# Performance work log

Measured on AMD Instinct MI355X. Metric: run time of the kernel, lower is better.

The kernel has to match this reference:

```python
import jax, jax.numpy as jnp
import numpy as np

HEAD_NUM = 16
EMBED_DIM = 1024
HIDDEN_DIM = 1024
HEAD_DIM = HIDDEN_DIM // HEAD_NUM


def setup_inputs() -> dict:
    key = jax.random.key(0)
    ks = jax.random.split(key, 7)
    B, S = 2, 2048
    X = jax.random.normal(ks[0], (B, S, EMBED_DIM), dtype=jnp.float32)
    sc = 1.0 / np.sqrt(EMBED_DIM)
    Wq = jax.random.normal(ks[1], (EMBED_DIM, HIDDEN_DIM), dtype=jnp.float32) * sc
    Wk = jax.random.normal(ks[2], (EMBED_DIM, HIDDEN_DIM), dtype=jnp.float32) * sc
    Wv = jax.random.normal(ks[3], (EMBED_DIM, HIDDEN_DIM), dtype=jnp.float32) * sc
    bq = jax.random.normal(ks[4], (HIDDEN_DIM,), dtype=jnp.float32) * 0.01
    bk = jax.random.normal(ks[5], (HIDDEN_DIM,), dtype=jnp.float32) * 0.01
    bv = jax.random.normal(ks[6], (HIDDEN_DIM,), dtype=jnp.float32) * 0.01
    return {"X": X, "Wq": Wq, "bq": bq, "Wk": Wk, "bk": bk, "Wv": Wv, "bv": bv}


def reference(X, Wq, bq, Wk, bk, Wv, bv):
    B, S, _ = X.shape
    # projections -> [B, H, S, D]
    def split_heads(t):
        return t.reshape(B, S, HEAD_NUM, HEAD_DIM).transpose(0, 2, 1, 3)
    Q = split_heads(X @ Wq + bq)
    K = split_heads(X @ Wk + bk)  # computed but unused, faithful to source bug
    V = split_heads(X @ Wv + bv)
    # NOTE: source computes Q @ V^T (bug), reproduced faithfully
    scores = jnp.einsum('bhqd,bhkd->bhqk', Q, V) / np.sqrt(HEAD_DIM)
    attn = jax.nn.softmax(scores, axis=-1)  # dropout is identity in eval
    out = jnp.einsum('bhqk,bhkd->bhqd', attn, V)
    return out.transpose(0, 2, 1, 3).reshape(B, S, HIDDEN_DIM)
```

## Files before the change

kernel.cpp:

```cpp
#include <hip/hip_runtime.h>
#include <math.h>


constexpr int BATCH = 2;
constexpr int SEQ   = 2048;
constexpr int EMB   = 1024;
constexpr int NHEAD = 16;
constexpr int HDIM  = 64;
constexpr int HID   = 1024;

typedef __attribute__((ext_vector_type(8))) _Float16 half8;
typedef __attribute__((ext_vector_type(4))) float    f32x4;

#define MFMA16(a, b, c) __builtin_amdgcn_mfma_f32_16x16x32_f16((a), (b), (c), 0, 0, 0)

constexpr int LDT = 80;

__device__ __forceinline__ _Float16 f2h(float f) { return (_Float16)f; }

__global__ __launch_bounds__(256) void conv_x_kernel(
    const float* __restrict__ X, _Float16* __restrict__ Xb, int n4)
{
    union Pack { uint2 q; _Float16 e[4]; };
    int idx = blockIdx.x * 256 + threadIdx.x;
    int stride = gridDim.x * 256;
    for (int i = idx; i < n4; i += stride) {
        float4 v = ((const float4*)X)[i];
        Pack p;
        p.e[0] = f2h(v.x); p.e[1] = f2h(v.y);
        p.e[2] = f2h(v.z); p.e[3] = f2h(v.w);
        ((uint2*)Xb)[i] = p.q;
    }
}

__global__ __launch_bounds__(256) void conv_wt_kernel(
    const float* __restrict__ W, _Float16* __restrict__ WT)
{
    __shared__ _Float16 T[64 * 68];
    const int tid = threadIdx.x;
    const int n0 = blockIdx.x * 64;
    const int k0 = blockIdx.y * 64;

    #pragma unroll
    for (int i = 0; i < 4; ++i) {
        const int u = tid + i * 256;
        const int r = u >> 4;
        const int c4 = (u & 15) << 2;
        const float4 v = *(const float4*)&W[(size_t)(k0 + r) * HID + n0 + c4];
        T[r * 68 + c4 + 0] = f2h(v.x);
        T[r * 68 + c4 + 1] = f2h(v.y);
        T[r * 68 + c4 + 2] = f2h(v.z);
        T[r * 68 + c4 + 3] = f2h(v.w);
    }
    __syncthreads();

    union Pack { uint4 q; _Float16 e[8]; };
    #pragma unroll
    for (int i = 0; i < 2; ++i) {
        const int u = tid + i * 256;
        const int n = u >> 3;
        const int kc = (u & 7) << 3;
        Pack p;
        #pragma unroll
        for (int j = 0; j < 8; ++j) p.e[j] = T[(kc + j) * 68 + n];
        *(uint4*)&WT[(size_t)(n0 + n) * EMB + k0 + kc] = p.q;
    }
}

__global__ __launch_bounds__(256) void proj_kernel(
    const _Float16* __restrict__ Xb, const _Float16* __restrict__ WTq,
    const _Float16* __restrict__ WTv, const float* __restrict__ bq,
    const float* __restrict__ bv, _Float16* __restrict__ Qo,
    _Float16* __restrict__ Vo, _Float16* __restrict__ VTo)
{
    __shared__ __align__(16) _Float16 Xs[128 * LDT];
    __shared__ __align__(16) _Float16 Wqs[64 * LDT];
    __shared__ __align__(16) _Float16 Wvs[64 * LDT];

    const int tid  = threadIdx.x;
    const int lane = tid & 63;
    const int w    = tid >> 6;
    const int wg   = blockIdx.x;
    const int nid  = (wg & 7) * 64 + (wg >> 3);
    const int h    = nid >> 5;
    const int m0   = (nid & 31) * 128;
    const int n0   = h * HDIM;
    const int l15  = lane & 15;
    const int l4   = lane >> 4;

    f32x4 aq[2][4], av[2][4];
    #pragma unroll
    for (int mt = 0; mt < 2; ++mt)
        #pragma unroll
        for (int nt = 0; nt < 4; ++nt) {
            aq[mt][nt] = f32x4{0.f, 0.f, 0.f, 0.f};
            av[mt][nt] = f32x4{0.f, 0.f, 0.f, 0.f};
        }

    for (int k0 = 0; k0 < EMB; k0 += 64) {
        #pragma unroll
        for (int i = 0; i < 4; ++i) {
            const int u = tid + i * 256;
            const int r = u >> 3;
            const int c8 = (u & 7) << 3;
            *(uint4*)&Xs[r * LDT + c8] =
                *(const uint4*)&Xb[(size_t)(m0 + r) * EMB + k0 + c8];
        }
        #pragma unroll
        for (int i = 0; i < 2; ++i) {
            const int u = tid + i * 256;
            const int r = u >> 3;
            const int c8 = (u & 7) << 3;
            *(uint4*)&Wqs[r * LDT + c8] =
                *(const uint4*)&WTq[(size_t)(n0 + r) * EMB + k0 + c8];
            *(uint4*)&Wvs[r * LDT + c8] =
                *(const uint4*)&WTv[(size_t)(n0 + r) * EMB + k0 + c8];
        }
        __syncthreads();

        __builtin_amdgcn_s_setprio(1);
        #pragma unroll
        for (int kd = 0; kd < 2; ++kd) {
            const int ko = kd * 32 + l4 * 8;
            half8 xa0 = *(const half8*)&Xs[(w * 32 + l15) * LDT + ko];
            half8 xa1 = *(const half8*)&Xs[(w * 32 + 16 + l15) * LDT + ko];
            #pragma unroll
            for (int nt = 0; nt < 4; ++nt) {
                half8 wq = *(const half8*)&Wqs[(nt * 16 + l15) * LDT + ko];
                half8 wv = *(const half8*)&Wvs[(nt * 16 + l15) * LDT + ko];
                aq[0][nt] = MFMA16(xa0, wq, aq[0][nt]);
                aq[1][nt] = MFMA16(xa1, wq, aq[1][nt]);
                av[0][nt] = MFMA16(xa0, wv, av[0][nt]);
                av[1][nt] = MFMA16(xa1, wv, av[1][nt]);
            }
        }
        __builtin_amdgcn_s_setprio(0);
        __syncthreads();
    }

    #pragma unroll
    for (int nt = 0; nt < 4; ++nt) {
        const int d = nt * 16 + l15;
        const float bqv = bq[n0 + d];
        const float bvv = bv[n0 + d];
        #pragma unroll
        for (int mt = 0; mt < 2; ++mt)
            #pragma unroll
            for (int r = 0; r < 4; ++r) {
                const int m = m0 + w * 32 + mt * 16 + l4 * 4 + r;
                const int bb = m >> 11;
                const int s  = m & (SEQ - 1);
                const int bh = bb * NHEAD + h;
                const float vval = av[mt][nt][r] + bvv;
                Qo[((size_t)bh * SEQ + s) * HDIM + d] = f2h(aq[mt][nt][r] + bqv);
                Vo[((size_t)bh * SEQ + s) * HDIM + d] = f2h(vval);
                VTo[((size_t)bh * HDIM + d) * SEQ + s] = f2h(vval);
            }
    }
}

__global__ __launch_bounds__(256) void attn_kernel(
    const _Float16* __restrict__ Qw, const _Float16* __restrict__ Vw,
    const _Float16* __restrict__ VTw, float* __restrict__ out)
{
    __shared__ __align__(16) _Float16 PQs[64 * LDT];
    __shared__ __align__(16) _Float16 Vs[64 * LDT];
    __shared__ __align__(16) _Float16 VTs[64 * LDT];

    const int tid  = threadIdx.x;
    const int lane = tid & 63;
    const int w    = tid >> 6;
    const int l15  = lane & 15;
    const int l4   = lane >> 4;
    const int wg = blockIdx.x;
    const int nw = (wg & 7) * 128 + (wg >> 3);
    const int bh = nw >> 5;
    const int qb = nw & 31;
    const int b  = bh >> 4;
    const int h  = bh & (NHEAD - 1);
    const int s0 = qb * 64;

    const _Float16* Qp  = Qw  + (size_t)bh * SEQ * HDIM;
    const _Float16* Vp  = Vw  + (size_t)bh * SEQ * HDIM;
    const _Float16* VTp = VTw + (size_t)bh * HDIM * SEQ;

    auto stageV = [&](int t) {
        #pragma unroll
        for (int i = 0; i < 2; ++i) {
            const int u = tid + i * 256;
            const int r = u >> 3;
            const int c8 = (u & 7) << 3;
            *(uint4*)&Vs[r * LDT + c8] =
                *(const uint4*)&Vp[(size_t)(t * 64 + r) * HDIM + c8];
            *(uint4*)&VTs[r * LDT + c8] =
                *(const uint4*)&VTp[(size_t)r * SEQ + t * 64 + c8];
        }
    };

    #pragma unroll
    for (int i = 0; i < 2; ++i) {
        const int u = tid + i * 256;
        const int r = u >> 3;
        const int c8 = (u & 7) << 3;
        *(uint4*)&PQs[r * LDT + c8] =
            *(const uint4*)&Qp[(size_t)(s0 + r) * HDIM + c8];
    }
    stageV(0);
    __syncthreads();

    const half8 qa0 = *(const half8*)&PQs[(w * 16 + l15) * LDT + l4 * 8];
    const half8 qa1 = *(const half8*)&PQs[(w * 16 + l15) * LDT + 32 + l4 * 8];

    f32x4 acc_o[4];
    #pragma unroll
    for (int dt = 0; dt < 4; ++dt) acc_o[dt] = f32x4{0.f, 0.f, 0.f, 0.f};
    float m_i[4] = {-INFINITY, -INFINITY, -INFINITY, -INFINITY};
    float l_i[4] = {0.f, 0.f, 0.f, 0.f};

    const int chi  = l15 >> 3;
    const int hl   = l15 & 7;
    const int rkey = l15 & 7;

    for (int t = 0; t < SEQ / 64; ++t) {
        f32x4 acc_s[4];
        #pragma unroll
        for (int nt = 0; nt < 4; ++nt) acc_s[nt] = f32x4{0.f, 0.f, 0.f, 0.f};
        __builtin_amdgcn_s_setprio(1);
        #pragma unroll
        for (int nt = 0; nt < 4; ++nt) {
            half8 vb0 = *(const half8*)&Vs[(nt * 16 + l15) * LDT + l4 * 8];
            half8 vb1 = *(const half8*)&Vs[(nt * 16 + l15) * LDT + 32 + l4 * 8];
            acc_s[nt] = MFMA16(qa0, vb0, acc_s[nt]);
            acc_s[nt] = MFMA16(qa1, vb1, acc_s[nt]);
        }
        __builtin_amdgcn_s_setprio(0);

        #pragma unroll
        for (int r = 0; r < 4; ++r) {
            float sA = acc_s[0][r] * 0.125f;
            float sB = acc_s[1][r] * 0.125f;
            float sC = acc_s[2][r] * 0.125f;
            float sD = acc_s[3][r] * 0.125f;
            float mloc = fmaxf(fmaxf(sA, sB), fmaxf(sC, sD));
            #pragma unroll
            for (int off = 1; off < 16; off <<= 1)
                mloc = fmaxf(mloc, __shfl_xor(mloc, off));
            const float mnew = fmaxf(m_i[r], mloc);
            const float corr = __expf(m_i[r] - mnew);
            const float p0 = __expf(sA - mnew);
            const float p1 = __expf(sB - mnew);
            const float p2 = __expf(sC - mnew);
            const float p3 = __expf(sD - mnew);
            float rs = (p0 + p1) + (p2 + p3);
            #pragma unroll
            for (int off = 1; off < 16; off <<= 1)
                rs += __shfl_xor(rs, off);
            l_i[r] = l_i[r] * corr + rs;
            m_i[r] = mnew;
            const int key = (l4 * 4 + r) & 7;
            _Float16* pr = &PQs[(w * 16 + l4 * 4 + r) * LDT];
            pr[(((0 + chi) ^ key) << 3) + hl] = f2h(p0);
            pr[(((2 + chi) ^ key) << 3) + hl] = f2h(p1);
            pr[(((4 + chi) ^ key) << 3) + hl] = f2h(p2);
            pr[(((6 + chi) ^ key) << 3) + hl] = f2h(p3);
            acc_o[0][r] *= corr; acc_o[1][r] *= corr;
            acc_o[2][r] *= corr; acc_o[3][r] *= corr;
        }

        const _Float16* prd = &PQs[(w * 16 + l15) * LDT];
        half8 pa0 = *(const half8*)&prd[((l4 ^ rkey) << 3)];
        half8 pa1 = *(const half8*)&prd[(((4 + l4) ^ rkey) << 3)];
        __builtin_amdgcn_s_setprio(1);
        #pragma unroll
        for (int dt = 0; dt < 4; ++dt) {
            half8 vt0 = *(const half8*)&VTs[(dt * 16 + l15) * LDT + l4 * 8];
            half8 vt1 = *(const half8*)&VTs[(dt * 16 + l15) * LDT + 32 + l4 * 8];
            acc_o[dt] = MFMA16(pa0, vt0, acc_o[dt]);
            acc_o[dt] = MFMA16(pa1, vt1, acc_o[dt]);
        }
        __builtin_amdgcn_s_setprio(0);

        __syncthreads();
        if (t + 1 < SEQ / 64) {
            stageV(t + 1);
            __syncthreads();
        }
    }

    #pragma unroll
    for (int r = 0; r < 4; ++r) {
        const float inv = 1.f / l_i[r];
        const int s = s0 + w * 16 + l4 * 4 + r;
        float* op = &out[((size_t)(b * SEQ + s)) * HID + h * HDIM + l15];
        op[ 0] = acc_o[0][r] * inv;
        op[16] = acc_o[1][r] * inv;
        op[32] = acc_o[2][r] * inv;
        op[48] = acc_o[3][r] * inv;
    }
}

extern "C" void kernel_launch(void* const* d_in, const int* in_sizes, int n_in,
                              void* d_out, int out_size, void* d_ws, size_t ws_size,
                              hipStream_t stream) {
    (void)in_sizes; (void)n_in; (void)out_size; (void)ws_size;
    const float* X  = (const float*)d_in[0];
    const float* Wq = (const float*)d_in[1];
    const float* bq = (const float*)d_in[2];
    const float* Wv = (const float*)d_in[5];
    const float* bv = (const float*)d_in[6];
    float* outp = (float*)d_out;

    char* ws = (char*)d_ws;
    _Float16* Xb  = (_Float16*)(ws);
    _Float16* WTq = (_Float16*)(ws + (8u  << 20));
    _Float16* WTv = (_Float16*)(ws + (10u << 20));
    _Float16* Qb  = (_Float16*)(ws + (12u << 20));
    _Float16* Vb  = (_Float16*)(ws + (20u << 20));
    _Float16* VTb = (_Float16*)(ws + (28u << 20));

    conv_x_kernel<<<2048, 256, 0, stream>>>(X, Xb, (BATCH * SEQ * EMB) / 4);
    conv_wt_kernel<<<dim3(16, 16), 256, 0, stream>>>(Wq, WTq);
    conv_wt_kernel<<<dim3(16, 16), 256, 0, stream>>>(Wv, WTv);
    proj_kernel<<<512, 256, 0, stream>>>(Xb, WTq, WTv, bq, bv, Qb, Vb, VTb);
    attn_kernel<<<1024, 256, 0, stream>>>(Qb, Vb, VTb, outp);
}
```

Before: 218.5 us.

## Prefetch tiles via registers, lazy softmax rescale, MFMA row-sum, LDS-transposed V store

Both the projection and attention kernels now prefetch the next global tile into registers while the current tile is being computed, so load latency overlaps MFMA work. The projection epilogue writes V^T through an LDS transpose, giving coalesced 16-byte stores in place of strided scalar ones. Attention switches to exp2 with a folded log2e scale and only rescales the accumulator when the running max grows past a threshold. The softmax denominator now comes from an extra MFMA column of ones rather than shuffle reductions, and the conv_x grid is halved. This trades extra registers and one more MFMA tile per step for less latency, shuffle and exp work, with some risk to occupancy.

```diff
diff --git a/kernel.cpp b/kernel.cpp
--- a/kernel.cpp
+++ b/kernel.cpp
@@ -15,6 +15,9 @@
 #define MFMA16(a, b, c) __builtin_amdgcn_mfma_f32_16x16x32_f16((a), (b), (c), 0, 0, 0)
 
 constexpr int LDT = 80;
+
+#define QK_SCALE 0.18033688011112042f
+#define LOG2_THR 11.0f
 
 __device__ __forceinline__ _Float16 f2h(float f) { return (_Float16)f; }
 
@@ -97,26 +100,40 @@
             av[mt][nt] = f32x4{0.f, 0.f, 0.f, 0.f};
         }
 
+    uint4 rx[4], rwq[2], rwv[2];
+    auto issueP = [&](int k0) {
+        #pragma unroll
+        for (int i = 0; i < 4; ++i) {
+            const int u = tid + i * 256, r = u >> 3, c8 = (u & 7) << 3;
+            rx[i] = *(const uint4*)&Xb[(size_t)(m0 + r) * EMB + k0 + c8];
+        }
+        #pragma unroll
+        for (int i = 0; i < 2; ++i) {
+            const int u = tid + i * 256, r = u >> 3, c8 = (u & 7) << 3;
+            rwq[i] = *(const uint4*)&WTq[(size_t)(n0 + r) * EMB + k0 + c8];
+            rwv[i] = *(const uint4*)&WTv[(size_t)(n0 + r) * EMB + k0 + c8];
+        }
+    };
+    auto writeP = [&]() {
+        #pragma unroll
+        for (int i = 0; i < 4; ++i) {
+            const int u = tid + i * 256, r = u >> 3, c8 = (u & 7) << 3;
+            *(uint4*)&Xs[r * LDT + c8] = rx[i];
+        }
+        #pragma unroll
+        for (int i = 0; i < 2; ++i) {
+            const int u = tid + i * 256, r = u >> 3, c8 = (u & 7) << 3;
+            *(uint4*)&Wqs[r * LDT + c8] = rwq[i];
+            *(uint4*)&Wvs[r * LDT + c8] = rwv[i];
+        }
+    };
+
+    issueP(0);
+    writeP();
+    __syncthreads();
+
     for (int k0 = 0; k0 < EMB; k0 += 64) {
-        #pragma unroll
-        for (int i = 0; i < 4; ++i) {
-            const int u = tid + i * 256;
-            const int r = u >> 3;
-            const int c8 = (u & 7) << 3;
-            *(uint4*)&Xs[r * LDT + c8] =
-                *(const uint4*)&Xb[(size_t)(m0 + r) * EMB + k0 + c8];
-        }
-        #pragma unroll
-        for (int i = 0; i < 2; ++i) {
-            const int u = tid + i * 256;
-            const int r = u >> 3;
-            const int c8 = (u & 7) << 3;
-            *(uint4*)&Wqs[r * LDT + c8] =
-                *(const uint4*)&WTq[(size_t)(n0 + r) * EMB + k0 + c8];
-            *(uint4*)&Wvs[r * LDT + c8] =
-                *(const uint4*)&WTv[(size_t)(n0 + r) * EMB + k0 + c8];
-        }
-        __syncthreads();
+        if (k0 + 64 < EMB) issueP(k0 + 64);
 
         __builtin_amdgcn_s_setprio(1);
         #pragma unroll
@@ -136,7 +153,15 @@
         }
         __builtin_amdgcn_s_setprio(0);
         __syncthreads();
-    }
+        if (k0 + 64 < EMB) writeP();
+        __syncthreads();
+    }
+
+    constexpr int LV = 65;
+    _Float16* Vlds = Xs;
+    const int bb = m0 >> 11;
+    const int s_base = m0 & (SEQ - 1);
+    const int bh = bb * NHEAD + h;
 
     #pragma unroll
     for (int nt = 0; nt < 4; ++nt) {
@@ -147,15 +172,27 @@
         for (int mt = 0; mt < 2; ++mt)
             #pragma unroll
             for (int r = 0; r < 4; ++r) {
-                const int m = m0 + w * 32 + mt * 16 + l4 * 4 + r;
-                const int bb = m >> 11;
-                const int s  = m & (SEQ - 1);
-                const int bh = bb * NHEAD + h;
-                const float vval = av[mt][nt][r] + bvv;
-                Qo[((size_t)bh * SEQ + s) * HDIM + d] = f2h(aq[mt][nt][r] + bqv);
-                Vo[((size_t)bh * SEQ + s) * HDIM + d] = f2h(vval);
-                VTo[((size_t)bh * HDIM + d) * SEQ + s] = f2h(vval);
+                const int sl = w * 32 + mt * 16 + l4 * 4 + r;
+                const int s  = s_base + sl;
+                const _Float16 qh = f2h(aq[mt][nt][r] + bqv);
+                const _Float16 vh = f2h(av[mt][nt][r] + bvv);
+                Qo[((size_t)bh * SEQ + s) * HDIM + d] = qh;
+                Vo[((size_t)bh * SEQ + s) * HDIM + d] = vh;
+                Vlds[sl * LV + d] = vh;
             }
+    }
+    __syncthreads();
+
+    union PK { uint4 q; _Float16 e[8]; };
+    #pragma unroll
+    for (int i = 0; i < 4; ++i) {
+        const int c  = tid + i * 256;
+        const int d  = c >> 4;
+        const int sc = (c & 15) << 3;
+        PK p;
+        #pragma unroll
+        for (int j = 0; j < 8; ++j) p.e[j] = Vlds[(sc + j) * LV + d];
+        *(uint4*)&VTo[((size_t)bh * HDIM + d) * SEQ + s_base + sc] = p.q;
     }
 }
 
@@ -165,7 +202,7 @@
 {
     __shared__ __align__(16) _Float16 PQs[64 * LDT];
     __shared__ __align__(16) _Float16 Vs[64 * LDT];
-    __shared__ __align__(16) _Float16 VTs[64 * LDT];
+    __shared__ __align__(16) _Float16 VTs[80 * LDT];
 
     const int tid  = threadIdx.x;
     const int lane = tid & 63;
@@ -184,38 +221,47 @@
     const _Float16* Vp  = Vw  + (size_t)bh * SEQ * HDIM;
     const _Float16* VTp = VTw + (size_t)bh * HDIM * SEQ;
 
-    auto stageV = [&](int t) {
+    uint4 rv[2], rvt[2];
+    auto issueV = [&](int t) {
         #pragma unroll
         for (int i = 0; i < 2; ++i) {
-            const int u = tid + i * 256;
-            const int r = u >> 3;
-            const int c8 = (u & 7) << 3;
-            *(uint4*)&Vs[r * LDT + c8] =
-                *(const uint4*)&Vp[(size_t)(t * 64 + r) * HDIM + c8];
-            *(uint4*)&VTs[r * LDT + c8] =
-                *(const uint4*)&VTp[(size_t)r * SEQ + t * 64 + c8];
+            const int u = tid + i * 256, r = u >> 3, c8 = (u & 7) << 3;
+            rv[i]  = *(const uint4*)&Vp[(size_t)(t * 64 + r) * HDIM + c8];
+            rvt[i] = *(const uint4*)&VTp[(size_t)r * SEQ + t * 64 + c8];
         }
     };
+    auto writeV = [&]() {
+        #pragma unroll
+        for (int i = 0; i < 2; ++i) {
+            const int u = tid + i * 256, r = u >> 3, c8 = (u & 7) << 3;
+            *(uint4*)&Vs[r * LDT + c8]  = rv[i];
+            *(uint4*)&VTs[r * LDT + c8] = rvt[i];
+        }
+    };
 
     #pragma unroll
     for (int i = 0; i < 2; ++i) {
-        const int u = tid + i * 256;
-        const int r = u >> 3;
-        const int c8 = (u & 7) << 3;
+        const int u = tid + i * 256, r = u >> 3, c8 = (u & 7) << 3;
         *(uint4*)&PQs[r * LDT + c8] =
             *(const uint4*)&Qp[(size_t)(s0 + r) * HDIM + c8];
     }
-    stageV(0);
+    #pragma unroll
+    for (int i = 0; i < 5; ++i) {
+        const int idx = tid + i * 256;
+        if (idx < 16 * LDT)
+            VTs[64 * LDT + idx] = (idx < LDT) ? (_Float16)1.0f : (_Float16)0.0f;
+    }
+    issueV(0);
+    writeV();
     __syncthreads();
 
     const half8 qa0 = *(const half8*)&PQs[(w * 16 + l15) * LDT + l4 * 8];
     const half8 qa1 = *(const half8*)&PQs[(w * 16 + l15) * LDT + 32 + l4 * 8];
 
-    f32x4 acc_o[4];
-    #pragma unroll
-    for (int dt = 0; dt < 4; ++dt) acc_o[dt] = f32x4{0.f, 0.f, 0.f, 0.f};
+    f32x4 acc_o[5];
+    #pragma unroll
+    for (int dt = 0; dt < 5; ++dt) acc_o[dt] = f32x4{0.f, 0.f, 0.f, 0.f};
     float m_i[4] = {-INFINITY, -INFINITY, -INFINITY, -INFINITY};
-    float l_i[4] = {0.f, 0.f, 0.f, 0.f};
 
     const int chi  = l15 >> 3;
     const int hl   = l15 & 7;
@@ -235,36 +281,46 @@
         }
         __builtin_amdgcn_s_setprio(0);
 
+        if (t + 1 < SEQ / 64) issueV(t + 1);
+
+        float sc4[4][4], mloc[4];
+        int needf = 0;
         #pragma unroll
         for (int r = 0; r < 4; ++r) {
-            float sA = acc_s[0][r] * 0.125f;
-            float sB = acc_s[1][r] * 0.125f;
-            float sC = acc_s[2][r] * 0.125f;
-            float sD = acc_s[3][r] * 0.125f;
-            float mloc = fmaxf(fmaxf(sA, sB), fmaxf(sC, sD));
+            sc4[r][0] = acc_s[0][r] * QK_SCALE;
+            sc4[r][1] = acc_s[1][r] * QK_SCALE;
+            sc4[r][2] = acc_s[2][r] * QK_SCALE;
+            sc4[r][3] = acc_s[3][r] * QK_SCALE;
+            float ml = fmaxf(fmaxf(sc4[r][0], sc4[r][1]),
+                             fmaxf(sc4[r][2], sc4[r][3]));
             #pragma unroll
             for (int off = 1; off < 16; off <<= 1)
-                mloc = fmaxf(mloc, __shfl_xor(mloc, off));
-            const float mnew = fmaxf(m_i[r], mloc);
-            const float corr = __expf(m_i[r] - mnew);
-            const float p0 = __expf(sA - mnew);
-            const float p1 = __expf(sB - mnew);
-            const float p2 = __expf(sC - mnew);
-            const float p3 = __expf(sD - mnew);
-            float rs = (p0 + p1) + (p2 + p3);
+                ml = fmaxf(ml, __shfl_xor(ml, off));
+            mloc[r] = ml;
+            needf |= (ml > m_i[r] + LOG2_THR) ? 1 : 0;
+        }
+        if (__any(needf)) {
             #pragma unroll
-            for (int off = 1; off < 16; off <<= 1)
-                rs += __shfl_xor(rs, off);
-            l_i[r] = l_i[r] * corr + rs;
-            m_i[r] = mnew;
+            for (int r = 0; r < 4; ++r) {
+                const float mnew = fmaxf(m_i[r], mloc[r]);
+                const float corr = __builtin_amdgcn_exp2f(m_i[r] - mnew);
+                m_i[r] = mnew;
+                #pragma unroll
+                for (int dt = 0; dt < 5; ++dt) acc_o[dt][r] *= corr;
+            }
+        }
+        #pragma unroll
+        for (int r = 0; r < 4; ++r) {
+            const float p0 = __builtin_amdgcn_exp2f(sc4[r][0] - m_i[r]);
+            const float p1 = __builtin_amdgcn_exp2f(sc4[r][1] - m_i[r]);
+            const float p2 = __builtin_amdgcn_exp2f(sc4[r][2] - m_i[r]);
+            const float p3 = __builtin_amdgcn_exp2f(sc4[r][3] - m_i[r]);
             const int key = (l4 * 4 + r) & 7;
             _Float16* pr = &PQs[(w * 16 + l4 * 4 + r) * LDT];
             pr[(((0 + chi) ^ key) << 3) + hl] = f2h(p0);
             pr[(((2 + chi) ^ key) << 3) + hl] = f2h(p1);
             pr[(((4 + chi) ^ key) << 3) + hl] = f2h(p2);
             pr[(((6 + chi) ^ key) << 3) + hl] = f2h(p3);
-            acc_o[0][r] *= corr; acc_o[1][r] *= corr;
-            acc_o[2][r] *= corr; acc_o[3][r] *= corr;
         }
 
         const _Float16* prd = &PQs[(w * 16 + l15) * LDT];
@@ -272,7 +328,7 @@
         half8 pa1 = *(const half8*)&prd[(((4 + l4) ^ rkey) << 3)];
         __builtin_amdgcn_s_setprio(1);
         #pragma unroll
-        for (int dt = 0; dt < 4; ++dt) {
+        for (int dt = 0; dt < 5; ++dt) {
             half8 vt0 = *(const half8*)&VTs[(dt * 16 + l15) * LDT + l4 * 8];
             half8 vt1 = *(const half8*)&VTs[(dt * 16 + l15) * LDT + 32 + l4 * 8];
             acc_o[dt] = MFMA16(pa0, vt0, acc_o[dt]);
@@ -281,15 +337,14 @@
         __builtin_amdgcn_s_setprio(0);
 
         __syncthreads();
-        if (t + 1 < SEQ / 64) {
-            stageV(t + 1);
-            __syncthreads();
-        }
+        if (t + 1 < SEQ / 64) writeV();
+        __syncthreads();
     }
 
     #pragma unroll
     for (int r = 0; r < 4; ++r) {
-        const float inv = 1.f / l_i[r];
+        const float ls  = __shfl(acc_o[4][r], (lane & 48));
+        const float inv = 1.f / ls;
         const int s = s0 + w * 16 + l4 * 4 + r;
         float* op = &out[((size_t)(b * SEQ + s)) * HID + h * HDIM + l15];
         op[ 0] = acc_o[0][r] * inv;
@@ -318,7 +373,7 @@
     _Float16* Vb  = (_Float16*)(ws + (20u << 20));
     _Float16* VTb = (_Float16*)(ws + (28u << 20));
 
-    conv_x_kernel<<<2048, 256, 0, stream>>>(X, Xb, (BATCH * SEQ * EMB) / 4);
+    conv_x_kernel<<<1024, 256, 0, stream>>>(X, Xb, (BATCH * SEQ * EMB) / 4);
     conv_wt_kernel<<<dim3(16, 16), 256, 0, stream>>>(Wq, WTq);
     conv_wt_kernel<<<dim3(16, 16), 256, 0, stream>>>(Wv, WTv);
     proj_kernel<<<512, 256, 0, stream>>>(Xb, WTq, WTv, bq, bv, Qb, Vb, VTb);
```

Result: slower. 324.3 us (+48.4%).
